# Optimization experiments

Hardware: AMD Instinct MI355X
Metric: run time of the kernel (lower is better)

## Reference

```python
import jax, jax.numpy as jnp
import numpy as np

H = 512          # hidden_size
HALF = 256       # hidden_size // 2 (RGCN feature dim)
NHEAD = 8
NLAYER = 12
NBLOCK = 2
NENT = 50000
NREL = 12
NBASES = 8
NEDGE = 500000
TXTD = 768       # raw text/image feature dim
BATCH, ELEN, SLEN = 32, 50, 128


def setup_inputs() -> dict:
    key = jax.random.key(0)
    ks = jax.random.split(key, 40)
    def p(i, shape, scale=0.02):
        return jax.random.normal(ks[i], shape, jnp.float32) * scale
    inp = {
        'entity_ids': jax.random.randint(ks[0], (BATCH, ELEN), 0, NENT),
        'token_embeds': jax.random.normal(ks[1], (BATCH, SLEN, H), jnp.float32),
        'edge_index': jax.random.randint(ks[2], (2, NEDGE), 0, NENT),
        'edge_type': jax.random.randint(ks[3], (NEDGE,), 0, NREL),
        'node_embeds': p(4, (NENT, HALF)),
        'rgcn_basis': p(5, (NBASES, HALF, HALF)),
        'rgcn_comp': p(6, (NREL, NBASES), 0.3),
        'rgcn_root': p(7, (HALF, HALF)),
        'rgcn_bias': p(8, (HALF,)),
        'kg_proj_w': p(9, (HALF, H)), 'kg_proj_b': p(10, (H,)),
        'text_proj_w': p(11, (TXTD, H)), 'text_proj_b': p(12, (H,)),
        'image_proj_w': p(13, (TXTD, H)), 'image_proj_b': p(14, (H,)),
        'cq_w': p(15, (H, H)), 'cq_b': p(16, (H,)),
        'kgk_w': p(17, (H, H)), 'kgk_b': p(18, (H,)),
        'imk_w': p(19, (H, H)), 'imk_b': p(20, (H,)),
        'txk_w': p(21, (H, H)), 'txk_b': p(22, (H,)),
        'pp1_w1': p(23, (H, HALF)), 'pp1_b1': p(24, (HALF,)),
        'pp1_w2': p(25, (HALF, H)), 'pp1_b2': p(26, (H,)),
        'pp2_w': p(27, (H, NLAYER * NBLOCK * H)), 'pp2_b': p(28, (NLAYER * NBLOCK * H,)),
        'text_embeds_init': p(29, (NENT, TXTD), 1.0),
        'image_embeds_init': p(30, (NENT, TXTD), 1.0),
    }
    return inp


def _rgcn(x, edge_index, edge_type, basis, comp, root, bias):
    # PyG RGCNConv with basis decomposition, aggr='mean', root weight + bias.
    # mean_{e: rel=r, dst=i}(x[src_e] @ W_r) == (mean_{e}(x[src_e])) @ W_r, so we
    # aggregate raw features per (dst, relation) segment then apply W_r once per node.
    N = x.shape[0]
    src, dst = edge_index[0], edge_index[1]
    seg = dst * NREL + edge_type                      # combined (node, relation) key
    msgs = x[src]                                     # [E, HALF] gather
    agg = jax.ops.segment_sum(msgs, seg, num_segments=N * NREL)
    cnt = jax.ops.segment_sum(jnp.ones((src.shape[0],), x.dtype), seg, num_segments=N * NREL)
    mean = (agg / jnp.maximum(cnt, 1.0)[:, None]).reshape(N, NREL, HALF)
    w_rel = jnp.einsum('rb,bio->rio', comp, basis)    # [R, HALF, HALF]
    out = jnp.einsum('nri,rio->no', mean, w_rel) + x @ root + bias
    return out


def reference(entity_ids, token_embeds, edge_index, edge_type, node_embeds,
              rgcn_basis, rgcn_comp, rgcn_root, rgcn_bias,
              kg_proj_w, kg_proj_b, text_proj_w, text_proj_b,
              image_proj_w, image_proj_b, cq_w, cq_b,
              kgk_w, kgk_b, imk_w, imk_b, txk_w, txk_b,
              pp1_w1, pp1_b1, pp1_w2, pp1_b2, pp2_w, pp2_b,
              text_embeds_init, image_embeds_init):
    kg_all = _rgcn(node_embeds, edge_index, edge_type, rgcn_basis, rgcn_comp, rgcn_root, rgcn_bias)
    kg_all = kg_all @ kg_proj_w + kg_proj_b           # [N, H]
    kg_feat = kg_all[entity_ids]                      # [B, L, H]
    text_feat = text_embeds_init[entity_ids] @ text_proj_w + text_proj_b
    image_feat = image_embeds_init[entity_ids] @ image_proj_w + image_proj_b
    # context-guided fusion
    q = (jnp.mean(token_embeds, axis=1) @ cq_w + cq_b)[:, None, :]   # [B, 1, H]
    kg_s = jnp.sum(q * (kg_feat @ kgk_w + kgk_b), -1, keepdims=True)
    img_s = jnp.sum(q * (image_feat @ imk_w + imk_b), -1, keepdims=True)
    txt_s = jnp.sum(q * (text_feat @ txk_w + txk_b), -1, keepdims=True)
    w = jax.nn.softmax(jnp.concatenate([kg_s, img_s, txt_s], axis=-1), axis=-1)
    fused = w[..., 0:1] * kg_feat + w[..., 1:2] * image_feat + w[..., 2:3] * text_feat
    # prompt expansion
    h = jax.nn.relu(fused @ pp1_w1 + pp1_b1) @ pp1_w2 + pp1_b2 + fused
    p = h @ pp2_w + pp2_b                             # [B, L, NLAYER*NBLOCK*H]
    B, L = entity_ids.shape
    p = p.reshape(B, L, NLAYER, NBLOCK, NHEAD, H // NHEAD)
    p = jnp.transpose(p, (2, 3, 0, 4, 1, 5))          # [layer, block, B, head, L, head_dim]
    loss_cl = jnp.float32(0.0)                        # output_entity=False path
    return p, loss_cl
```

## Files before the change

kernel.cpp:

```cpp
#include <hip/hip_runtime.h>

#define HDIM 512
#define HALF 256
#define NRELS 12
#define NBASES 8
#define NLAYERS 12
#define NBLOCKS 2
#define NHEADS 8
#define NENTS 50000
#define TXTD 768
#define BATCH 32
#define ELEN 50
#define SLEN 128
#define NPOS (BATCH * ELEN)
#define NSEG (NPOS * NRELS)
#define BCAP 64

typedef unsigned short u16;
typedef __attribute__((ext_vector_type(8))) __bf16 bf16x8;
typedef __attribute__((ext_vector_type(4))) float f32x4;

__device__ __forceinline__ u16 f2bf(float f) {
    unsigned int u = __float_as_uint(f);
    unsigned int r = (u + 0x7FFFu + ((u >> 16) & 1u)) >> 16;
    return (u16)r;
}
__device__ __forceinline__ float bf2f(u16 v) {
    return __uint_as_float(((unsigned int)v) << 16);
}

#define ASYNC_COPY16(g, l)                                                              \
    __builtin_amdgcn_global_load_lds((const __attribute__((address_space(1))) void*)(g), \
                                     (__attribute__((address_space(3))) unsigned int*)(l), 16, 0, 0)

__global__ void init_kernel(int* __restrict__ map, int* __restrict__ segcnt,
                            int* __restrict__ nuniq, float* __restrict__ zb,
                            const float* __restrict__ kgb, const float* __restrict__ imb,
                            const float* __restrict__ txb, u16* __restrict__ SW,
                            const float* __restrict__ rgcn_bias,
                            const float* __restrict__ kg_proj_w,
                            const float* __restrict__ kg_proj_b,
                            float* __restrict__ biasC, float* __restrict__ out_last) {
    int blk = blockIdx.x;
    int t = threadIdx.x;
    if (blk >= 128) {
        int n = (blk - 128) * 256 + t;
        float acc = kg_proj_b[n];
        for (int c = 0; c < HALF; ++c) acc += rgcn_bias[c] * kg_proj_w[(size_t)c * HDIM + n];
        biasC[n] = acc;
        return;
    }
    int tid = blk * 256 + t;
    const int nt = 128 * 256;
    int4 m4 = {-1, -1, -1, -1};
    for (int i = tid; i < NENTS / 4; i += nt) ((int4*)map)[i] = m4;
    int4 z4 = {0, 0, 0, 0};
    for (int i = tid; i < NSEG / 4; i += nt) ((int4*)segcnt)[i] = z4;
    for (int i = tid; i < 2304; i += nt) zb[i] = 0.f;
    if (tid < HDIM) {
        SW[(size_t)1536 * HDIM + tid] = f2bf(kgb[tid]);
        SW[(size_t)1537 * HDIM + tid] = f2bf(imb[tid]);
        SW[(size_t)1538 * HDIM + tid] = f2bf(txb[tid]);
    }
    if (tid == 0) { *nuniq = 0; *out_last = 0.f; }
}

__global__ void dedup_kernel(const int* __restrict__ eid, int* __restrict__ map,
                             int* __restrict__ uniq, int* __restrict__ nuniq) {
    int i = blockIdx.x * blockDim.x + threadIdx.x;
    if (i >= NPOS) return;
    int n = eid[i];
    int old = atomicCAS(&map[n], -1, -2);
    if (old == -1) {
        int idx = atomicAdd(nuniq, 1);
        uniq[idx] = n;
        __threadfence();
        map[n] = idx;
    }
}

struct PrepArgs {
    const float* src[12];
    u16* dst[12];
};

__global__ __launch_bounds__(256) void midprep_kernel(
    const float* __restrict__ tok, u16* __restrict__ TMEAN,
    const int* __restrict__ uniq, const int* __restrict__ nuniq,
    const float* __restrict__ txi, const float* __restrict__ imi,
    u16* __restrict__ TXIN, u16* __restrict__ IMIN,
    const int* __restrict__ ei, const int* __restrict__ et, const int* __restrict__ map,
    int* __restrict__ segcnt, int* __restrict__ bucket, int E, PrepArgs a) {
    int blk = blockIdx.x;
    int t = threadIdx.x;
    if (blk < 64) {
        int b = blk >> 1;
        int col = (blk & 1) * 256 + t;
        float s = 0.f;
        for (int si = 0; si < SLEN; ++si) s += tok[((size_t)b * SLEN + si) * HDIM + col];
        TMEAN[(size_t)b * HDIM + col] = f2bf(s * (1.0f / SLEN));
    } else if (blk < 352) {
        if (t >= TXTD / 4) return;
        int nu = *nuniq;
        for (int u = blk - 64; u < NPOS; u += 288) {
            if (u >= nu) {
                ushort4 z = {0, 0, 0, 0};
                ((ushort4*)(TXIN + (size_t)u * TXTD))[t] = z;
                ((ushort4*)(IMIN + (size_t)u * TXTD))[t] = z;
                continue;
            }
            int n = uniq[u];
            float4 v = ((const float4*)(txi + (size_t)n * TXTD))[t];
            ushort4 o;
            o.x = f2bf(v.x); o.y = f2bf(v.y); o.z = f2bf(v.z); o.w = f2bf(v.w);
            ((ushort4*)(TXIN + (size_t)u * TXTD))[t] = o;
            v = ((const float4*)(imi + (size_t)n * TXTD))[t];
            o.x = f2bf(v.x); o.y = f2bf(v.y); o.z = f2bf(v.z); o.w = f2bf(v.w);
            ((ushort4*)(IMIN + (size_t)u * TXTD))[t] = o;
        }
    } else if (blk < 1024) {
        const int* __restrict__ dstA = ei + E;
        int tid0 = (blk - 352) * 256 + t;
        const int stride = 672 * 256;
        for (int e = tid0; e < E; e += stride) {
            int c = map[dstA[e]];
            if (c >= 0) {
                int seg = c * NRELS + et[e];
                int p = atomicAdd(&segcnt[seg], 1);
                if (p < BCAP) bucket[seg * BCAP + p] = ei[e];
            }
        }
    } else {
        constexpr int NN[7]  = {512, 512, 512, 256, 512, 12288, 512};
        constexpr int LDT[7] = {256, 768, 768, 512, 256, 512, 512};
        constexpr int BASE[13] = {0, 128, 512, 896, 1024, 1152, 7296,
                                  7552, 8064, 8128, 8384, 8640, 8896};
        __shared__ u16 tb[32][33];
        int bid = blk - 1024;
        int op = 0;
        #pragma unroll
        for (int i = 1; i < 12; ++i)
            if (bid >= BASE[i]) op = i;
        int idx = bid - BASE[op];
        if (op < 7) {
            int Nv = 0, ldt = 0;
            #pragma unroll
            for (int i = 0; i < 7; ++i)
                if (op == i) { Nv = NN[i]; ldt = LDT[i]; }
            int ncols = Nv / 32;
            int n0 = (idx % ncols) * 32, k0 = (idx / ncols) * 32;
            const float* W = a.src[op];
            u16* WT = a.dst[op];
            int tx = t & 31, ty = t >> 5;
            #pragma unroll
            for (int i = ty; i < 32; i += 8)
                tb[i][tx] = f2bf(W[(size_t)(k0 + i) * Nv + n0 + tx]);
            __syncthreads();
            #pragma unroll
            for (int i = ty; i < 32; i += 8)
                WT[(size_t)(n0 + i) * ldt + k0 + tx] = tb[tx][i];
        } else {
            int e = idx * 1024 + t * 4;
            float4 v = *(const float4*)(a.src[op] + e);
            ushort4 o;
            o.x = f2bf(v.x); o.y = f2bf(v.y); o.z = f2bf(v.z); o.w = f2bf(v.w);
            *(ushort4*)(a.dst[op] + e) = o;
        }
    }
}

template <int BM, int BN, int WM, int WN, bool SCATTER>
__device__ __forceinline__ void gemm_body(const u16* __restrict__ A, const u16* __restrict__ BT,
                                          const float* __restrict__ bias,
                                          void* __restrict__ Cout, int M, int N, int K,
                                          int bx, int by, bool outbf) {
    constexpr int MF = WM / 16, NF = WN / 16;
    constexpr int NWC = BN / WN;
    __shared__ u16 ldsA[BM][64];
    __shared__ u16 ldsB[BN][64];
    const int tid = threadIdx.x;
    const int lane = tid & 63;
    const int wv = tid >> 6;
    const int m0 = by * BM;
    const int n0 = bx * BN;
    const int wr = wv / NWC, wc = wv % NWC;
    const int srow = lane >> 3;
    const int sslot = lane & 7;

    f32x4 acc[MF][NF];
    #pragma unroll
    for (int i = 0; i < MF; ++i)
        #pragma unroll
        for (int j = 0; j < NF; ++j)
            #pragma unroll
            for (int r = 0; r < 4; ++r) acc[i][j][r] = 0.f;

    for (int k0 = 0; k0 < K; k0 += 64) {
        #pragma unroll
        for (int i = 0; i < BM / 32; ++i) {
            int R = wv * (BM / 4) + i * 8 + srow;
            int gm = m0 + R;
            gm = gm < M ? gm : M - 1;
            int s = sslot ^ (R & 7);
            ASYNC_COPY16(A + (size_t)gm * K + k0 + s * 8, &ldsA[wv * (BM / 4) + i * 8][0]);
        }
        #pragma unroll
        for (int i = 0; i < BN / 32; ++i) {
            int R = wv * (BN / 4) + i * 8 + srow;
            int s = sslot ^ (R & 7);
            ASYNC_COPY16(BT + (size_t)(n0 + R) * K + k0 + s * 8, &ldsB[wv * (BN / 4) + i * 8][0]);
        }
        __syncthreads();
        #pragma unroll
        for (int ks = 0; ks < 2; ++ks) {
            bf16x8 af[MF], bf[NF];
            int kg = ks * 4 + (lane >> 4);
            int rl = lane & 15;
            #pragma unroll
            for (int i = 0; i < MF; ++i) {
                int row = wr * WM + i * 16 + rl;
                af[i] = *(const bf16x8*)&ldsA[row][(kg ^ (row & 7)) * 8];
            }
            #pragma unroll
            for (int j = 0; j < NF; ++j) {
                int row = wc * WN + j * 16 + rl;
                bf[j] = *(const bf16x8*)&ldsB[row][(kg ^ (row & 7)) * 8];
            }
            #pragma unroll
            for (int i = 0; i < MF; ++i)
                #pragma unroll
                for (int j = 0; j < NF; ++j)
                    acc[i][j] = __builtin_amdgcn_mfma_f32_16x16x32_bf16(af[i], bf[j], acc[i][j], 0, 0, 0);
        }
        __syncthreads();
    }

    const int rl = lane & 15, rg = lane >> 4;
    #pragma unroll
    for (int i = 0; i < MF; ++i) {
        #pragma unroll
        for (int j = 0; j < NF; ++j) {
            int col = n0 + wc * WN + j * 16 + rl;
            float bv = bias[col];
            #pragma unroll
            for (int r = 0; r < 4; ++r) {
                int row = m0 + wr * WM + i * 16 + rg * 4 + r;
                if (row >= M) continue;
                float x = acc[i][j][r] + bv;
                if (SCATTER) {
                    int layer = col >> 10, blk = (col >> 9) & 1, head = (col >> 6) & 7, hd = col & 63;
                    int bb = row / ELEN, ll = row - bb * ELEN;
                    size_t oi = (((((size_t)layer * NBLOCKS + blk) * BATCH + bb) * NHEADS + head) * ELEN + ll) * 64 + hd;
                    ((float*)Cout)[oi] = x;
                } else if (outbf) {
                    ((u16*)Cout)[(size_t)row * N + col] = f2bf(x);
                } else {
                    ((float*)Cout)[(size_t)row * N + col] = x;
                }
            }
        }
    }
}

struct BuildArgs {
    const int *segcnt, *bucket, *uniq, *nuniq;
    const float *comp, *x;
    u16* MBX;
    const u16 *TMEAN, *CQT;
    const float* cq_b;
    u16* QB;
    const u16 *KGT, *W1f;
    const float* ZB;
    u16* WC;
    const u16 *TXIN, *TXT, *IMIN, *IMT;
    const float *txb, *imb;
    u16 *TXU, *IMU;
};
__global__ __launch_bounds__(256) void build_kernel(BuildArgs a) {
    int blk = blockIdx.x;
    if (blk >= NPOS) {
        const u16 *A, *BT;
        const float* bias;
        u16* C;
        int M, N, K, bx, by;
        if (blk >= NPOS + 8 + 288 + 200) {
            int i = blk - (NPOS + 8 + 288 + 200);
            A = a.IMIN; BT = a.IMT; bias = a.imb; C = a.IMU;
            M = NPOS; N = HDIM; K = TXTD; bx = i % 8; by = i / 8;
        } else if (blk >= NPOS + 8 + 288) {
            int i = blk - (NPOS + 8 + 288);
            A = a.TXIN; BT = a.TXT; bias = a.txb; C = a.TXU;
            M = NPOS; N = HDIM; K = TXTD; bx = i % 8; by = i / 8;
        } else if (blk >= NPOS + 8) {
            int i = blk - (NPOS + 8);
            A = a.KGT; BT = a.W1f; bias = a.ZB; C = a.WC;
            M = HDIM; N = 2304; K = HALF; bx = i % 36; by = i / 36;
        } else {
            A = a.TMEAN; BT = a.CQT; bias = a.cq_b; C = a.QB;
            M = BATCH; N = HDIM; K = HDIM; bx = blk - NPOS; by = 0;
        }
        gemm_body<64, 64, 32, 32, false>(A, BT, bias, C, M, N, K, bx, by, true);
        return;
    }
    int u = blk;
    int i = threadIdx.x;
    __shared__ float sc[NRELS * NBASES];
    if (i < NRELS * NBASES) sc[i] = a.comp[i];
    __syncthreads();
    u16* row = a.MBX + (size_t)u * 2304;
    int nu = *a.nuniq;
    if (u >= nu) {
        for (int b = 0; b < NBASES + 1; ++b) row[b * HALF + i] = 0;
        return;
    }
    float mr[NRELS];
    #pragma unroll
    for (int r = 0; r < NRELS; ++r) {
        int seg = u * NRELS + r;
        int c = a.segcnt[seg];
        int n = min(c, BCAP);
        float acc = 0.f;
        for (int e = 0; e < n; ++e) {
            int s = a.bucket[seg * BCAP + e];
            acc += a.x[(size_t)s * HALF + i];
        }
        mr[r] = acc * (1.f / fmaxf((float)c, 1.f));
    }
    #pragma unroll
    for (int b = 0; b < NBASES; ++b) {
        float v = 0.f;
        #pragma unroll
        for (int r = 0; r < NRELS; ++r) v += sc[r * NBASES + b] * mr[r];
        row[b * HALF + i] = f2bf(v);
    }
    row[NBASES * HALF + i] = f2bf(a.x[(size_t)a.uniq[u] * HALF + i]);
}

struct ProjArgs {
    const u16 *MBX, *WC, *QB, *SW;
    const float *biasC, *ZB;
    u16* KGU;
    float* QP;
};
__global__ __launch_bounds__(256) void proj_kernel(ProjArgs a) {
    int b = blockIdx.x;
    if (b < 200) {
        gemm_body<64, 64, 32, 32, false>(a.MBX, a.WC, a.biasC, a.KGU,
                                         NPOS, HDIM, 2304, b % 8, b / 8, true);
    } else {
        gemm_body<64, 64, 32, 32, false>(a.QB, a.SW, a.ZB, a.QP,
                                         BATCH, 1600, HDIM, b - 200, 0, false);
    }
}

__global__ __launch_bounds__(256) void tail_kernel(
    const int* __restrict__ eid, const int* __restrict__ map,
    const u16* __restrict__ KGU, const u16* __restrict__ IMU, const u16* __restrict__ TXU,
    const float* __restrict__ qp,
    const u16* __restrict__ W1T, const float* __restrict__ pp1_b1,
    const u16* __restrict__ W2T, const float* __restrict__ pp1_b2,
    u16* __restrict__ Hh) {
    __shared__ u16 FUS[16][520];
    __shared__ u16 P1s[16][264];
    const int bm0 = blockIdx.x * 16;
    const int lane = threadIdx.x & 63;
    const int wv = threadIdx.x >> 6;

    for (int rr = wv; rr < 16; rr += 4) {
        int bl = bm0 + rr;
        int b = bl / ELEN;
        int u = map[eid[bl]];
        const u16* kg = KGU + (size_t)u * HDIM;
        const u16* im = IMU + (size_t)u * HDIM;
        const u16* tx = TXU + (size_t)u * HDIM;
        const float* qrow = qp + (size_t)b * 1600;
        float pkg = 0.f, pim = 0.f, ptx = 0.f;
        for (int e = lane; e < HDIM; e += 64) {
            pkg += bf2f(kg[e]) * qrow[e];
            pim += bf2f(im[e]) * qrow[512 + e];
            ptx += bf2f(tx[e]) * qrow[1024 + e];
        }
        #pragma unroll
        for (int off = 32; off; off >>= 1) {
            pkg += __shfl_down(pkg, off);
            pim += __shfl_down(pim, off);
            ptx += __shfl_down(ptx, off);
        }
        float w0, w1, w2;
        if (lane == 0) {
            float av = pkg + qrow[1536];
            float c1 = pim + qrow[1537];
            float c2 = ptx + qrow[1538];
            float mx = fmaxf(av, fmaxf(c1, c2));
            float ea = __expf(av - mx), eb = __expf(c1 - mx), ec = __expf(c2 - mx);
            float inv = 1.f / (ea + eb + ec);
            w0 = ea * inv; w1 = eb * inv; w2 = ec * inv;
        }
        w0 = __shfl(w0, 0); w1 = __shfl(w1, 0); w2 = __shfl(w2, 0);
        for (int e = lane; e < HDIM; e += 64) {
            float v = w0 * bf2f(kg[e]) + w1 * bf2f(im[e]) + w2 * bf2f(tx[e]);
            FUS[rr][e] = f2bf(v);
        }
    }
    __syncthreads();

    {
        const int rl = lane & 15;
        const int kgrp = lane >> 4;
        f32x4 acc[4];
        #pragma unroll
        for (int j = 0; j < 4; ++j)
            #pragma unroll
            for (int r = 0; r < 4; ++r) acc[j][r] = 0.f;
        for (int kk = 0; kk < 512; kk += 32) {
            int k8 = kk + kgrp * 8;
            bf16x8 af = *(const bf16x8*)&FUS[rl][k8];
            bf16x8 bf[4];
            #pragma unroll
            for (int j = 0; j < 4; ++j) {
                int n = wv * 64 + j * 16 + rl;
                bf[j] = *(const bf16x8*)&W1T[(size_t)n * 512 + k8];
            }
            #pragma unroll
            for (int j = 0; j < 4; ++j)
                acc[j] = __builtin_amdgcn_mfma_f32_16x16x32_bf16(af, bf[j], acc[j], 0, 0, 0);
        }
        const int rg = lane >> 4;
        #pragma unroll
        for (int j = 0; j < 4; ++j) {
            int col = wv * 64 + j * 16 + rl;
            float bv = pp1_b1[col];
            #pragma unroll
            for (int r = 0; r < 4; ++r) {
                int row = rg * 4 + r;
                P1s[row][col] = f2bf(fmaxf(acc[j][r] + bv, 0.f));
            }
        }
    }
    __syncthreads();

    {
        const int rl = lane & 15;
        const int kgrp = lane >> 4;
        f32x4 acc[8];
        #pragma unroll
        for (int j = 0; j < 8; ++j)
            #pragma unroll
            for (int r = 0; r < 4; ++r) acc[j][r] = 0.f;
        for (int kk = 0; kk < 256; kk += 32) {
            int k8 = kk + kgrp * 8;
            bf16x8 af = *(const bf16x8*)&P1s[rl][k8];
            bf16x8 bf[8];
            #pragma unroll
            for (int j = 0; j < 8; ++j) {
                int n = wv * 128 + j * 16 + rl;
                bf[j] = *(const bf16x8*)&W2T[(size_t)n * 256 + k8];
            }
            #pragma unroll
            for (int j = 0; j < 8; ++j)
                acc[j] = __builtin_amdgcn_mfma_f32_16x16x32_bf16(af, bf[j], acc[j], 0, 0, 0);
        }
        const int rg = lane >> 4;
        #pragma unroll
        for (int j = 0; j < 8; ++j) {
            int col = wv * 128 + j * 16 + rl;
            float bv = pp1_b2[col];
            #pragma unroll
            for (int r = 0; r < 4; ++r) {
                int row = rg * 4 + r;
                float v = acc[j][r] + bv + bf2f(FUS[row][col]);
                Hh[(size_t)(bm0 + row) * HDIM + col] = f2bf(v);
            }
        }
    }
}

__global__ __launch_bounds__(256)
void pp2_kernel(const u16* __restrict__ A, const u16* __restrict__ BT,
                const float* __restrict__ bias, void* __restrict__ Cout,
                int M, int N, int K) {
    int id = blockIdx.x;
    int xcd = id & 7;
    int local = id >> 3;
    int bx = xcd * 12 + local % 12;
    int by = local / 12;
    gemm_body<128, 128, 64, 64, true>(A, BT, bias, Cout, M, N, K, bx, by, false);
}

extern "C" void kernel_launch(void* const* d_in, const int* in_sizes, int n_in,
                              void* d_out, int out_size, void* d_ws, size_t ws_size,
                              hipStream_t stream) {
    const int* entity_ids = (const int*)d_in[0];
    const float* token_embeds = (const float*)d_in[1];
    const int* edge_index = (const int*)d_in[2];
    const int* edge_type = (const int*)d_in[3];
    const float* node_embeds = (const float*)d_in[4];
    const float* rgcn_basis = (const float*)d_in[5];
    const float* rgcn_comp = (const float*)d_in[6];
    const float* rgcn_root = (const float*)d_in[7];
    const float* rgcn_bias = (const float*)d_in[8];
    const float* kg_proj_w = (const float*)d_in[9];
    const float* kg_proj_b = (const float*)d_in[10];
    const float* text_proj_w = (const float*)d_in[11];
    const float* text_proj_b = (const float*)d_in[12];
    const float* image_proj_w = (const float*)d_in[13];
    const float* image_proj_b = (const float*)d_in[14];
    const float* cq_w = (const float*)d_in[15];
    const float* cq_b = (const float*)d_in[16];
    const float* kgk_w = (const float*)d_in[17];
    const float* imk_w = (const float*)d_in[19];
    const float* txk_w = (const float*)d_in[21];
    const float* pp1_w1 = (const float*)d_in[23];
    const float* pp1_b1 = (const float*)d_in[24];
    const float* pp1_w2 = (const float*)d_in[25];
    const float* pp1_b2 = (const float*)d_in[26];
    const float* pp2_w = (const float*)d_in[27];
    const float* pp2_b = (const float*)d_in[28];
    const float* text_init = (const float*)d_in[29];
    const float* image_init = (const float*)d_in[30];

    const int E = in_sizes[3];

    size_t off = 0;
    auto alloc = [&](size_t bytes) { size_t o = off; off += (bytes + 255) & ~(size_t)255; return o; };
    char* ws = (char*)d_ws;
    size_t map_o  = alloc((size_t)NENTS * 4);
    size_t nun_o  = alloc(4);
    size_t unq_o  = alloc((size_t)NPOS * 4);
    size_t scnt_o = alloc((size_t)NSEG * 4);
    size_t bkt_o  = alloc((size_t)NSEG * BCAP * 4);
    size_t mbx_o  = alloc((size_t)NPOS * 2304 * 2);
    size_t w1f_o  = alloc((size_t)2304 * HALF * 2);
    size_t wc_o   = alloc((size_t)HDIM * 2304 * 2);
    size_t bc_o   = alloc((size_t)HDIM * 4);
    size_t kgt_o  = alloc((size_t)HDIM * HALF * 2);
    size_t kgu_o  = alloc((size_t)NPOS * HDIM * 2);
    size_t txin_o = alloc((size_t)NPOS * TXTD * 2);
    size_t imin_o = alloc((size_t)NPOS * TXTD * 2);
    size_t txt_o  = alloc((size_t)HDIM * TXTD * 2);
    size_t imt_o  = alloc((size_t)HDIM * TXTD * 2);
    size_t txu_o  = alloc((size_t)NPOS * HDIM * 2);
    size_t imu_o  = alloc((size_t)NPOS * HDIM * 2);
    size_t tm_o   = alloc((size_t)BATCH * HDIM * 2);
    size_t qb_o   = alloc((size_t)BATCH * HDIM * 2);
    size_t cqt_o  = alloc((size_t)HDIM * HDIM * 2);
    size_t sw_o   = alloc((size_t)1600 * HDIM * 2);
    size_t qp_o   = alloc((size_t)BATCH * 1600 * 4);
    size_t zb_o   = alloc((size_t)2304 * 4);
    size_t w1t_o  = alloc((size_t)HALF * HDIM * 2);
    size_t w2t_o  = alloc((size_t)HDIM * HALF * 2);
    size_t h_o    = alloc((size_t)NPOS * HDIM * 2);
    size_t pp2t_o = alloc((size_t)12288 * HDIM * 2);
    if (off > ws_size) return;

    int* map = (int*)(ws + map_o);
    int* nuniq = (int*)(ws + nun_o);
    int* uniq = (int*)(ws + unq_o);
    int* segcnt = (int*)(ws + scnt_o);
    int* bucket = (int*)(ws + bkt_o);
    u16* MBX = (u16*)(ws + mbx_o);
    u16* W1f = (u16*)(ws + w1f_o);
    u16* WC  = (u16*)(ws + wc_o);
    float* biasC = (float*)(ws + bc_o);
    u16* KGT = (u16*)(ws + kgt_o);
    u16* KGU = (u16*)(ws + kgu_o);
    u16* TXIN = (u16*)(ws + txin_o);
    u16* IMIN = (u16*)(ws + imin_o);
    u16* TXT = (u16*)(ws + txt_o);
    u16* IMT = (u16*)(ws + imt_o);
    u16* TXU = (u16*)(ws + txu_o);
    u16* IMU = (u16*)(ws + imu_o);
    u16* TMEAN = (u16*)(ws + tm_o);
    u16* QB  = (u16*)(ws + qb_o);
    u16* CQT = (u16*)(ws + cqt_o);
    u16* SW  = (u16*)(ws + sw_o);
    float* QP  = (float*)(ws + qp_o);
    float* ZB  = (float*)(ws + zb_o);
    u16* W1T = (u16*)(ws + w1t_o);
    u16* W2T = (u16*)(ws + w2t_o);
    u16* Hh  = (u16*)(ws + h_o);
    u16* PP2T = (u16*)(ws + pp2t_o);
    float* OUT = (float*)d_out;

    init_kernel<<<130, 256, 0, stream>>>(map, segcnt, nuniq, ZB,
                                         (const float*)d_in[18], (const float*)d_in[20],
                                         (const float*)d_in[22], SW,
                                         rgcn_bias, kg_proj_w, kg_proj_b, biasC,
                                         OUT + (out_size - 1));
    dedup_kernel<<<(NPOS + 255) / 256, 256, 0, stream>>>(entity_ids, map, uniq, nuniq);
    PrepArgs pa;
    pa.src[0] = kg_proj_w;    pa.dst[0] = KGT;
    pa.src[1] = text_proj_w;  pa.dst[1] = TXT;
    pa.src[2] = image_proj_w; pa.dst[2] = IMT;
    pa.src[3] = pp1_w1;       pa.dst[3] = W1T;
    pa.src[4] = pp1_w2;       pa.dst[4] = W2T;
    pa.src[5] = pp2_w;        pa.dst[5] = PP2T;
    pa.src[6] = cq_w;         pa.dst[6] = CQT;
    pa.src[7] = rgcn_basis;   pa.dst[7] = W1f;
    pa.src[8] = rgcn_root;    pa.dst[8] = W1f + (size_t)2048 * HALF;
    pa.src[9] = kgk_w;        pa.dst[9] = SW;
    pa.src[10] = imk_w;       pa.dst[10] = SW + (size_t)HDIM * HDIM;
    pa.src[11] = txk_w;       pa.dst[11] = SW + (size_t)2 * HDIM * HDIM;
    midprep_kernel<<<9920, 256, 0, stream>>>(token_embeds, TMEAN,
                                             uniq, nuniq, text_init, image_init, TXIN, IMIN,
                                             edge_index, edge_type, map, segcnt, bucket, E, pa);
    BuildArgs ba;
    ba.segcnt = segcnt; ba.bucket = bucket; ba.uniq = uniq; ba.nuniq = nuniq;
    ba.comp = rgcn_comp; ba.x = node_embeds; ba.MBX = MBX;
    ba.TMEAN = TMEAN; ba.CQT = CQT; ba.cq_b = cq_b; ba.QB = QB;
    ba.KGT = KGT; ba.W1f = W1f; ba.ZB = ZB; ba.WC = WC;
    ba.TXIN = TXIN; ba.TXT = TXT; ba.IMIN = IMIN; ba.IMT = IMT;
    ba.txb = text_proj_b; ba.imb = image_proj_b; ba.TXU = TXU; ba.IMU = IMU;
    build_kernel<<<NPOS + 8 + 288 + 400, 256, 0, stream>>>(ba);
    ProjArgs pr;
    pr.MBX = MBX; pr.WC = WC; pr.biasC = biasC; pr.KGU = KGU;
    pr.QB = QB; pr.SW = SW; pr.ZB = ZB; pr.QP = QP;
    proj_kernel<<<225, 256, 0, stream>>>(pr);
    tail_kernel<<<NPOS / 16, 256, 0, stream>>>(entity_ids, map, KGU, IMU, TXU, QP,
                                               W1T, pp1_b1, W2T, pp1_b2, Hh);
    pp2_kernel<<<1248, 256, 0, stream>>>(Hh, PP2T, pp2_b, OUT, NPOS, 12288, HDIM);
}
```

Measured before the change: 155.3 us.

## Vectorize edge bucketing, enlarge weight transpose tiles, drop pp2 XCD remap

The edge bucketing loop now uses one thread per four edges with int4 loads of destinations and types, replacing the grid-stride loop with a fixed 512-block range. Weight transpose/convert tiles grow from 32x32 to 64x64, which cuts the prep grid from 9920 to 4096 blocks. The pp2 GEMM also drops its XCD-aware block swizzle in favour of a plain 2D grid. Together these aim to lower launch and block-scheduling overhead in prep and to widen memory accesses. The trade-offs are a larger LDS tile with possible bank conflicts on the transposed reads, and the loss of the L2 locality the swizzle gave pp2.

After: 152.3 us (median of 2 runs). 1.02x faster.

```diff
diff --git a/kernel.cpp b/kernel.cpp
--- a/kernel.cpp
+++ b/kernel.cpp
@@ -118,25 +118,51 @@
             o.x = f2bf(v.x); o.y = f2bf(v.y); o.z = f2bf(v.z); o.w = f2bf(v.w);
             ((ushort4*)(IMIN + (size_t)u * TXTD))[t] = o;
         }
-    } else if (blk < 1024) {
+    } else if (blk < 864) {
         const int* __restrict__ dstA = ei + E;
-        int tid0 = (blk - 352) * 256 + t;
-        const int stride = 672 * 256;
-        for (int e = tid0; e < E; e += stride) {
-            int c = map[dstA[e]];
-            if (c >= 0) {
-                int seg = c * NRELS + et[e];
+        int gtid = (blk - 352) * 256 + t;
+        int e0 = gtid * 4;
+        if (e0 + 3 < E) {
+            int4 d4 = *(const int4*)(dstA + e0);
+            int4 t4 = *(const int4*)(et + e0);
+            int cc0 = map[d4.x], cc1 = map[d4.y], cc2 = map[d4.z], cc3 = map[d4.w];
+            if (cc0 >= 0) {
+                int seg = cc0 * NRELS + t4.x;
                 int p = atomicAdd(&segcnt[seg], 1);
-                if (p < BCAP) bucket[seg * BCAP + p] = ei[e];
+                if (p < BCAP) bucket[seg * BCAP + p] = ei[e0];
+            }
+            if (cc1 >= 0) {
+                int seg = cc1 * NRELS + t4.y;
+                int p = atomicAdd(&segcnt[seg], 1);
+                if (p < BCAP) bucket[seg * BCAP + p] = ei[e0 + 1];
+            }
+            if (cc2 >= 0) {
+                int seg = cc2 * NRELS + t4.z;
+                int p = atomicAdd(&segcnt[seg], 1);
+                if (p < BCAP) bucket[seg * BCAP + p] = ei[e0 + 2];
+            }
+            if (cc3 >= 0) {
+                int seg = cc3 * NRELS + t4.w;
+                int p = atomicAdd(&segcnt[seg], 1);
+                if (p < BCAP) bucket[seg * BCAP + p] = ei[e0 + 3];
+            }
+        } else {
+            for (int e = e0; e < E; ++e) {
+                int c = map[dstA[e]];
+                if (c >= 0) {
+                    int seg = c * NRELS + et[e];
+                    int p = atomicAdd(&segcnt[seg], 1);
+                    if (p < BCAP) bucket[seg * BCAP + p] = ei[e];
+                }
             }
         }
     } else {
         constexpr int NN[7]  = {512, 512, 512, 256, 512, 12288, 512};
         constexpr int LDT[7] = {256, 768, 768, 512, 256, 512, 512};
-        constexpr int BASE[13] = {0, 128, 512, 896, 1024, 1152, 7296,
-                                  7552, 8064, 8128, 8384, 8640, 8896};
-        __shared__ u16 tb[32][33];
-        int bid = blk - 1024;
+        constexpr int BASE[13] = {0, 32, 128, 224, 256, 288, 1824,
+                                  1888, 2400, 2464, 2720, 2976, 3232};
+        __shared__ u16 tb[64][65];
+        int bid = blk - 864;
         int op = 0;
         #pragma unroll
         for (int i = 1; i < 12; ++i)
@@ -147,18 +173,22 @@
             #pragma unroll
             for (int i = 0; i < 7; ++i)
                 if (op == i) { Nv = NN[i]; ldt = LDT[i]; }
-            int ncols = Nv / 32;
-            int n0 = (idx % ncols) * 32, k0 = (idx / ncols) * 32;
+            int ncols = Nv >> 6;
+            int n0 = (idx % ncols) * 64, k0 = (idx / ncols) * 64;
             const float* W = a.src[op];
             u16* WT = a.dst[op];
-            int tx = t & 31, ty = t >> 5;
-            #pragma unroll
-            for (int i = ty; i < 32; i += 8)
-                tb[i][tx] = f2bf(W[(size_t)(k0 + i) * Nv + n0 + tx]);
+            int lane = t & 63, wv = t >> 6;
+            #pragma unroll
+            for (int i2 = 0; i2 < 16; ++i2) {
+                int r = wv * 16 + i2;
+                tb[r][lane] = f2bf(W[(size_t)(k0 + r) * Nv + n0 + lane]);
+            }
             __syncthreads();
             #pragma unroll
-            for (int i = ty; i < 32; i += 8)
-                WT[(size_t)(n0 + i) * ldt + k0 + tx] = tb[tx][i];
+            for (int i2 = 0; i2 < 16; ++i2) {
+                int rr = wv * 16 + i2;
+                WT[(size_t)(n0 + rr) * ldt + k0 + lane] = tb[lane][rr];
+            }
         } else {
             int e = idx * 1024 + t * 4;
             float4 v = *(const float4*)(a.src[op] + e);
@@ -479,12 +509,7 @@
 void pp2_kernel(const u16* __restrict__ A, const u16* __restrict__ BT,
                 const float* __restrict__ bias, void* __restrict__ Cout,
                 int M, int N, int K) {
-    int id = blockIdx.x;
-    int xcd = id & 7;
-    int local = id >> 3;
-    int bx = xcd * 12 + local % 12;
-    int by = local / 12;
-    gemm_body<128, 128, 64, 64, true>(A, BT, bias, Cout, M, N, K, bx, by, false);
+    gemm_body<128, 128, 64, 64, true>(A, BT, bias, Cout, M, N, K, blockIdx.x, blockIdx.y, false);
 }
 
 extern "C" void kernel_launch(void* const* d_in, const int* in_sizes, int n_in,
@@ -601,7 +626,7 @@
     pa.src[9] = kgk_w;        pa.dst[9] = SW;
     pa.src[10] = imk_w;       pa.dst[10] = SW + (size_t)HDIM * HDIM;
     pa.src[11] = txk_w;       pa.dst[11] = SW + (size_t)2 * HDIM * HDIM;
-    midprep_kernel<<<9920, 256, 0, stream>>>(token_embeds, TMEAN,
+    midprep_kernel<<<4096, 256, 0, stream>>>(token_embeds, TMEAN,
                                              uniq, nuniq, text_init, image_init, TXIN, IMIN,
                                              edge_index, edge_type, map, segcnt, bucket, E, pa);
     BuildArgs ba;
@@ -618,5 +643,6 @@
     proj_kernel<<<225, 256, 0, stream>>>(pr);
     tail_kernel<<<NPOS / 16, 256, 0, stream>>>(entity_ids, map, KGU, IMU, TXU, QP,
                                                W1T, pp1_b1, W2T, pp1_b2, Hh);
-    pp2_kernel<<<1248, 256, 0, stream>>>(Hh, PP2T, pp2_b, OUT, NPOS, 12288, HDIM);
-}
+    pp2_kernel<<<dim3(12288 / 128, (NPOS + 127) / 128), 256, 0, stream>>>(
+        Hh, PP2T, pp2_b, OUT, NPOS, 12288, HDIM);
+}
```
